# Kernel optimization log

Measured on AMD Instinct MI355X. Metric: run time of the kernel, lower is better.

The kernel has to match this reference:

```python
import jax, jax.numpy as jnp
import numpy as np

NUM_SLOTS = 8
DIM = 256
ITERS = 3
EPS_LN = 1e-5

def _ln(x, g, b):
    mu = jnp.mean(x, axis=-1, keepdims=True)
    var = jnp.var(x, axis=-1, keepdims=True)
    return (x - mu) * jax.lax.rsqrt(var + EPS_LN) * g + b

def setup_inputs() -> dict:
    key = jax.random.key(0)
    ks = jax.random.split(key, 16)
    d = DIM
    s = 1.0 / np.sqrt(d)
    inp = {
        'x': jax.random.normal(ks[0], (64, 4096, d), jnp.float32),
        'noise': jax.random.normal(ks[1], (64, NUM_SLOTS, d), jnp.float32),
        'slots_mu': jax.random.normal(ks[2], (1, 1, d), jnp.float32),
        'slots_logsigma': jnp.zeros((1, 1, d), jnp.float32),
        'Wq': jax.random.uniform(ks[3], (d, d), jnp.float32, -s, s),
        'Wk': jax.random.uniform(ks[4], (d, d), jnp.float32, -s, s),
        'Wv': jax.random.uniform(ks[5], (d, d), jnp.float32, -s, s),
        'W_ih': jax.random.uniform(ks[6], (3 * d, d), jnp.float32, -s, s),
        'W_hh': jax.random.uniform(ks[7], (3 * d, d), jnp.float32, -s, s),
        'b_ih': jax.random.uniform(ks[8], (3 * d,), jnp.float32, -s, s),
        'b_hh': jax.random.uniform(ks[9], (3 * d,), jnp.float32, -s, s),
        'W1': jax.random.uniform(ks[10], (d, d), jnp.float32, -s, s),
        'b1': jax.random.uniform(ks[11], (d,), jnp.float32, -s, s),
        'W2': jax.random.uniform(ks[12], (d, d), jnp.float32, -s, s),
        'b2': jax.random.uniform(ks[13], (d,), jnp.float32, -s, s),
        'g_in': jnp.ones((d,), jnp.float32), 'be_in': jnp.zeros((d,), jnp.float32),
        'g_sl': jnp.ones((d,), jnp.float32), 'be_sl': jnp.zeros((d,), jnp.float32),
        'g_ff': jnp.ones((d,), jnp.float32), 'be_ff': jnp.zeros((d,), jnp.float32),
    }
    return inp

def _gru(x, h, W_ih, W_hh, b_ih, b_hh):
    # torch.nn.GRUCell math; x,h: [M, d]
    gi = x @ W_ih.T + b_ih
    gh = h @ W_hh.T + b_hh
    i_r, i_z, i_n = jnp.split(gi, 3, axis=-1)
    h_r, h_z, h_n = jnp.split(gh, 3, axis=-1)
    r = jax.nn.sigmoid(i_r + h_r)
    z = jax.nn.sigmoid(i_z + h_z)
    n = jnp.tanh(i_n + r * h_n)
    return (1.0 - z) * n + z * h

def reference(x, noise, slots_mu, slots_logsigma, Wq, Wk, Wv, W_ih, W_hh, b_ih, b_hh,
              W1, b1, W2, b2, g_in, be_in, g_sl, be_sl, g_ff, be_ff):
    B, N, d = x.shape
    scale = d ** (-0.5)
    x = _ln(x, g_in, be_in)
    slots = slots_mu + noise * jnp.exp(slots_logsigma)  # [B, K, d]
    # k/v are loop-invariant; hoist (same math as original)
    k = jnp.einsum('bnd,ed->bne', x, Wk)
    v = jnp.einsum('bnd,ed->bne', x, Wv)
    for _ in range(ITERS):
        slots_prev = slots
        q = jnp.einsum('bkd,ed->bke', _ln(slots, g_sl, be_sl), Wq)
        attn = jax.nn.softmax(jnp.einsum('bkd,bnd->bkn', q, k) * scale, axis=-1) + 1e-8
        attn = attn / jnp.sum(attn, axis=-1, keepdims=True)
        updates = jnp.einsum('bkn,bnd->bkd', attn, v)
        slots = _gru(updates.reshape(-1, d), slots_prev.reshape(-1, d),
                     W_ih, W_hh, b_ih, b_hh).reshape(B, NUM_SLOTS, d)
        h = jax.nn.relu(jnp.einsum('bkd,ed->bke', _ln(slots, g_ff, be_ff), W1) + b1)
        slots = slots + jnp.einsum('bkd,ed->bke', h, W2) + b2
    return slots.reshape(B, NUM_SLOTS * d)
```

## Files before the change

### kernel.cpp

```cpp
#include <hip/hip_runtime.h>
#include <cstddef>

#define DIM 256
#define NSLOT 8
#define BATCH 64
#define NTOK 4096
#define SEGB 16
#define NPART SEGB
#define ITERS 3
#define EPS 1e-5f

typedef short bf16x8 __attribute__((ext_vector_type(8)));
typedef short bf16x4 __attribute__((ext_vector_type(4)));
typedef float f32x4  __attribute__((ext_vector_type(4)));

static __device__ __forceinline__ short f2bf(float f) {
    union { float f; unsigned u; } v; v.f = f;
    unsigned r = v.u + 0x7fffu + ((v.u >> 16) & 1u);
    return (short)(r >> 16);
}

enum : size_t {
    OFF_M     = 0,
    OFF_WIHT  = OFF_M    + 256 * 256,
    OFF_WHHT  = OFF_WIHT + 256 * 768,
    OFF_WVT   = OFF_WHHT + 256 * 768,
    OFF_W1T   = OFF_WVT  + 256 * 256,
    OFF_W2T   = OFF_W1T  + 256 * 256,
    OFF_SLOTS = OFF_W2T  + 256 * 256,
    OFF_SNEW  = OFF_SLOTS + BATCH * NSLOT * 256,
    OFF_QT    = OFF_SNEW  + BATCH * NSLOT * 256,
    OFF_H     = OFF_QT    + BATCH * NSLOT * 256,
    OFF_UPD   = OFF_H     + BATCH * NSLOT * 256,
    OFF_UPART = OFF_UPD   + BATCH * NSLOT * 256,
    OFF_LPART = OFF_UPART + (size_t)BATCH * NPART * NSLOT * 256,
    OFF_XLN   = OFF_LPART + BATCH * NPART * 16,
    OFF_XLT   = OFF_XLN   + (size_t)BATCH * NTOK * 128,
    WS_FLOATS = OFF_XLT   + (size_t)BATCH * NTOK * 128
};

__global__ __launch_bounds__(256) void k_transpose(const float* __restrict__ w_ih,
                                                   const float* __restrict__ w_hh,
                                                   const float* __restrict__ wv,
                                                   const float* __restrict__ w1,
                                                   const float* __restrict__ w2,
                                                   float* __restrict__ ws) {
    int z = blockIdx.z;
    const float* src;
    float* dst;
    int R;
    if (z == 0)      { src = w_ih; dst = ws + OFF_WIHT; R = 768; }
    else if (z == 1) { src = w_hh; dst = ws + OFF_WHHT; R = 768; }
    else if (z == 2) { src = wv;   dst = ws + OFF_WVT;  R = 256; }
    else if (z == 3) { src = w1;   dst = ws + OFF_W1T;  R = 256; }
    else             { src = w2;   dst = ws + OFF_W2T;  R = 256; }
    if ((int)blockIdx.x * 32 >= R) return;
    __shared__ float tile[32][33];
    int lx = threadIdx.x & 31, ly = threadIdx.x >> 5;
    int r0 = blockIdx.x * 32, c0 = blockIdx.y * 32;
#pragma unroll
    for (int p = 0; p < 4; ++p)
        tile[ly + p * 8][lx] = src[(size_t)(r0 + ly + p * 8) * 256 + c0 + lx];
    __syncthreads();
#pragma unroll
    for (int p = 0; p < 4; ++p)
        dst[(size_t)(c0 + ly + p * 8) * R + r0 + lx] = tile[lx][ly + p * 8];
}

__global__ __launch_bounds__(256) void k_m(const float* __restrict__ wq,
                                           const float* __restrict__ wk,
                                           float* __restrict__ ws) {
    int d = blockIdx.x, t = threadIdx.x;
    float acc = 0.f;
    for (int e = 0; e < 256; ++e)
        acc += wq[e * 256 + d] * wk[e * 256 + t];
    ws[OFF_M + d * 256 + t] = acc * 0.0625f;
}

__global__ __launch_bounds__(256) void k_init(const float* __restrict__ mu,
                                              const float* __restrict__ logsig,
                                              const float* __restrict__ noise,
                                              float* __restrict__ ws) {
    int i = blockIdx.x * 256 + threadIdx.x;
    int d = i & 255;
    ws[OFF_SLOTS + i] = mu[d] + noise[i] * __expf(logsig[d]);
}

__global__ __launch_bounds__(256) void k_prep(const float* __restrict__ x,
                                              const float* __restrict__ g_in,
                                              const float* __restrict__ be_in,
                                              float* __restrict__ ws) {
    int seg = blockIdx.x, b = blockIdx.y;
    int t = threadIdx.x;
    int w = t >> 6, lane = t & 63;
    int q = lane >> 4, s16 = lane & 15;

    __shared__ short xT[256 * 64];
    __shared__ float gl[256], bl[256];
    gl[t] = g_in[t];
    bl[t] = be_in[t];
    __syncthreads();

    short* xln = (short*)(ws + OFF_XLN);
    short* xlt = (short*)(ws + OFF_XLT);
    int g0 = ((w * 16 + s16) >> 3);
    int t7 = s16 & 7;

    for (int tt = 0; tt < 4; ++tt) {
        int tok = seg * 256 + tt * 64 + w * 16 + s16;
        const float4* xp = (const float4*)(x + ((size_t)b * NTOK + tok) * 256 + q * 8);
        float4 xa[8], xb[8];
#pragma unroll
        for (int i = 0; i < 8; ++i) { xa[i] = xp[8 * i]; xb[i] = xp[8 * i + 1]; }
        float s1 = 0.f, s2 = 0.f;
#pragma unroll
        for (int i = 0; i < 8; ++i) {
            s1 += xa[i].x + xa[i].y + xa[i].z + xa[i].w + xb[i].x + xb[i].y + xb[i].z + xb[i].w;
            s2 += xa[i].x * xa[i].x + xa[i].y * xa[i].y + xa[i].z * xa[i].z + xa[i].w * xa[i].w
                + xb[i].x * xb[i].x + xb[i].y * xb[i].y + xb[i].z * xb[i].z + xb[i].w * xb[i].w;
        }
        s1 += __shfl_xor(s1, 16); s2 += __shfl_xor(s2, 16);
        s1 += __shfl_xor(s1, 32); s2 += __shfl_xor(s2, 32);
        float mu = s1 * (1.f / 256.f);
        float rstd = rsqrtf(s2 * (1.f / 256.f) - mu * mu + EPS);

        bf16x8 af[8];
#pragma unroll
        for (int i = 0; i < 8; ++i) {
            int dbase = i * 32 + q * 8;
            float4 gA = *(const float4*)&gl[dbase];
            float4 gB = *(const float4*)&gl[dbase + 4];
            float4 bA = *(const float4*)&bl[dbase];
            float4 bB = *(const float4*)&bl[dbase + 4];
            bf16x8 f;
            f[0] = f2bf((xa[i].x - mu) * rstd * gA.x + bA.x);
            f[1] = f2bf((xa[i].y - mu) * rstd * gA.y + bA.y);
            f[2] = f2bf((xa[i].z - mu) * rstd * gA.z + bA.z);
            f[3] = f2bf((xa[i].w - mu) * rstd * gA.w + bA.w);
            f[4] = f2bf((xb[i].x - mu) * rstd * gB.x + bB.x);
            f[5] = f2bf((xb[i].y - mu) * rstd * gB.y + bB.y);
            f[6] = f2bf((xb[i].z - mu) * rstd * gB.z + bB.z);
            f[7] = f2bf((xb[i].w - mu) * rstd * gB.w + bB.w);
            af[i] = f;
        }

        short* xrow = xln + ((size_t)b * NTOK + tok) * 256;
#pragma unroll
        for (int i = 0; i < 8; ++i)
            *(bf16x8*)&xrow[i * 32 + q * 8] = af[i];

        __syncthreads();

#pragma unroll
        for (int i = 0; i < 8; ++i) {
            int Ki = (4 * i + q) & 7;
            int dbase = i * 32 + q * 8;
            bf16x8 f = af[i];
#pragma unroll
            for (int e = 0; e < 8; ++e) {
                int gp = (g0 ^ e ^ Ki) & 7;
                xT[((dbase + e) << 6) + (gp << 3) + t7] = f[e];
            }
        }
        __syncthreads();

        short* xtb = xlt + (size_t)(b * 64 + seg * 4 + tt) * 256 * 64;
#pragma unroll
        for (int c = 0; c < 4; ++c) {
            int d = (4 * w + c) * 16 + s16;
            int swz = (d ^ (d >> 3)) & 7;
            const short* row = &xT[d << 6];
            bf16x8 b0 = *(const bf16x8*)&row[((q ^ swz) & 7) << 3];
            bf16x8 b1 = *(const bf16x8*)&row[(((4 + q) ^ swz) & 7) << 3];
            *(bf16x8*)&xtb[d * 64 + q * 8] = b0;
            *(bf16x8*)&xtb[d * 64 + (q + 4) * 8] = b1;
        }
    }
}

__global__ __launch_bounds__(256) void k_qt(float* __restrict__ ws,
                                            const float* __restrict__ g_sl,
                                            const float* __restrict__ be_sl) {
    __shared__ float ln[2048];
    int chunk = blockIdx.x, b = blockIdx.y;
    int t = threadIdx.x, wave = t >> 6, lane = t & 63;
    const float* slots = ws + OFF_SLOTS + b * 2048;
    float4 gf = ((const float4*)g_sl)[lane];
    float4 bf = ((const float4*)be_sl)[lane];
#pragma unroll
    for (int rr = 0; rr < 2; ++rr) {
        int r = wave + rr * 4;
        float4 v = ((const float4*)(slots + r * 256))[lane];
        float s1 = v.x + v.y + v.z + v.w;
        float s2 = v.x * v.x + v.y * v.y + v.z * v.z + v.w * v.w;
#pragma unroll
        for (int m = 1; m < 64; m <<= 1) { s1 += __shfl_xor(s1, m); s2 += __shfl_xor(s2, m); }
        float mu = s1 * (1.f / 256.f);
        float rstd = rsqrtf(s2 * (1.f / 256.f) - mu * mu + EPS);
        float4 o;
        o.x = (v.x - mu) * rstd * gf.x + bf.x;
        o.y = (v.y - mu) * rstd * gf.y + bf.y;
        o.z = (v.z - mu) * rstd * gf.z + bf.z;
        o.w = (v.w - mu) * rstd * gf.w + bf.w;
        *((float4*)&ln[r * 256 + lane * 4]) = o;
    }
    __syncthreads();
    const float* M = ws + OFF_M;
    int k0 = t >> 6;
    int e = chunk * 64 + (t & 63);
    float a0 = 0.f, a1 = 0.f;
    for (int d = 0; d < 256; ++d) {
        float m = M[d * 256 + e];
        a0 += ln[k0 * 256 + d] * m;
        a1 += ln[(k0 + 4) * 256 + d] * m;
    }
    float* qt = ws + OFF_QT + b * 2048;
    qt[k0 * 256 + e] = a0;
    qt[(k0 + 4) * 256 + e] = a1;
}

__global__ __launch_bounds__(256) void k_attn(float* __restrict__ ws) {
    int seg = blockIdx.x, b = blockIdx.y;
    int t = threadIdx.x;
    int w = t >> 6, lane = t & 63;
    int q = lane >> 4, s16 = lane & 15;

    __shared__ short qhi[16 * 264];
    __shared__ short Etmp[2][16 * 72];
    __shared__ float lsum[4][8];

    const float* qtg = ws + OFF_QT + b * 2048;
    for (int idx = t; idx < 16 * 264; idx += 256) {
        int s = idx / 264, d = idx - s * 264;
        qhi[idx] = (s < 8 && d < 256) ? f2bf(qtg[s * 256 + d]) : (short)0;
    }
    __syncthreads();

    bf16x8 qf[8];
#pragma unroll
    for (int i = 0; i < 8; ++i)
        qf[i] = *(const bf16x8*)&qhi[s16 * 264 + i * 32 + q * 8];

    f32x4 U[4];
#pragma unroll
    for (int c = 0; c < 4; ++c) U[c] = (f32x4){0.f, 0.f, 0.f, 0.f};
    float lacc = 0.f;

    const short* xln = (const short*)(ws + OFF_XLN);
    const short* xlt = (const short*)(ws + OFF_XLT);
    int mytok = seg * 256 + w * 16 + s16;

    for (int tt = 0; tt < 4; ++tt) {
        const short* xr = xln + ((size_t)b * NTOK + mytok + tt * 64) * 256 + q * 8;
        bf16x8 af[8];
#pragma unroll
        for (int i = 0; i < 8; ++i) af[i] = *(const bf16x8*)&xr[i * 32];

        f32x4 Lc = (f32x4){0.f, 0.f, 0.f, 0.f};
#pragma unroll
        for (int i = 0; i < 8; ++i)
            Lc = __builtin_amdgcn_mfma_f32_16x16x32_bf16(af[i], qf[i], Lc, 0, 0, 0);

        bf16x4 e2;
#pragma unroll
        for (int r = 0; r < 4; ++r) {
            float E = __expf(fminf(Lc[r], 30.f));
            lacc += E;
            e2[r] = f2bf(E);
        }
        *(bf16x4*)&Etmp[tt & 1][s16 * 72 + w * 16 + q * 4] = e2;
        __syncthreads();

        bf16x8 ea0 = *(const bf16x8*)&Etmp[tt & 1][s16 * 72 + q * 8];
        bf16x8 ea1 = *(const bf16x8*)&Etmp[tt & 1][s16 * 72 + 32 + q * 8];

        const short* xtb = xlt + (size_t)(b * 64 + seg * 4 + tt) * 256 * 64;
#pragma unroll
        for (int c = 0; c < 4; ++c) {
            int d = (4 * w + c) * 16 + s16;
            bf16x8 b0 = *(const bf16x8*)&xtb[d * 64 + q * 8];
            bf16x8 b1 = *(const bf16x8*)&xtb[d * 64 + (q + 4) * 8];
            U[c] = __builtin_amdgcn_mfma_f32_16x16x32_bf16(ea0, b0, U[c], 0, 0, 0);
            U[c] = __builtin_amdgcn_mfma_f32_16x16x32_bf16(ea1, b1, U[c], 0, 0, 0);
        }
    }

    lacc += __shfl_xor(lacc, 16); lacc += __shfl_xor(lacc, 32);
    __syncthreads();
    if (q == 0 && s16 < 8) lsum[w][s16] = lacc;
    __syncthreads();
    float* lpart = ws + OFF_LPART + (size_t)(b * NPART + seg) * 16;
    if (t < 8) lpart[t] = lsum[0][t] + lsum[1][t] + lsum[2][t] + lsum[3][t];
    float* up = ws + OFF_UPART + (size_t)(b * NPART + seg) * NSLOT * 256;
#pragma unroll
    for (int c = 0; c < 4; ++c) {
        int d = (4 * w + c) * 16 + s16;
#pragma unroll
        for (int r = 0; r < 4; ++r) {
            int slot = q * 4 + r;
            if (slot < 8) up[slot * 256 + d] = U[c][r];
        }
    }
}

static __device__ __forceinline__ void ln_row2(const float* src, float* dst,
                                               const float* __restrict__ g,
                                               const float* __restrict__ be,
                                               int wave, int lane) {
    if (wave < 2) {
        float4 v = *(const float4*)(src + wave * 256 + lane * 4);
        float s1 = v.x + v.y + v.z + v.w;
        float s2 = v.x * v.x + v.y * v.y + v.z * v.z + v.w * v.w;
#pragma unroll
        for (int m = 1; m < 64; m <<= 1) { s1 += __shfl_xor(s1, m); s2 += __shfl_xor(s2, m); }
        float mu = s1 * (1.f / 256.f);
        float rstd = rsqrtf(s2 * (1.f / 256.f) - mu * mu + EPS);
        float4 gf = ((const float4*)g)[lane];
        float4 bf = ((const float4*)be)[lane];
        float4 o;
        o.x = (v.x - mu) * rstd * gf.x + bf.x;
        o.y = (v.y - mu) * rstd * gf.y + bf.y;
        o.z = (v.z - mu) * rstd * gf.z + bf.z;
        o.w = (v.w - mu) * rstd * gf.w + bf.w;
        *(float4*)(dst + wave * 256 + lane * 4) = o;
    }
}

__global__ __launch_bounds__(512) void k_fused(float* __restrict__ ws,
                                               const float* __restrict__ b_ih,
                                               const float* __restrict__ b_hh,
                                               const float* __restrict__ g_ff,
                                               const float* __restrict__ be_ff,
                                               const float* __restrict__ b1p,
                                               const float* __restrict__ b2p,
                                               const float* __restrict__ g_sl,
                                               const float* __restrict__ be_sl,
                                               float* __restrict__ dout) {
    __shared__ __align__(16) float uc[2][256], upd[2][256], sl[2][256], snew[2][256];
    __shared__ __align__(16) float lnb[2][256], hbuf[2][256], so[2][256];
    __shared__ float lsv[2];

    int sp = blockIdx.x, b = blockIdx.y, t = threadIdx.x;
    int s0 = sp * 2;
    int s = t >> 8, d = t & 255;
    int wave = t >> 6, lane = t & 63;

    if (t < 32) {
        int ss = t >> 4, g = t & 15;
        float lv = ws[OFF_LPART + (size_t)(b * NPART + g) * 16 + s0 + ss];
#pragma unroll
        for (int m = 1; m < 16; m <<= 1) lv += __shfl_xor(lv, m);
        if ((t & 15) == 0) lsv[ss] = lv;
    }

    const float* up0 = ws + OFF_UPART + (size_t)b * NPART * NSLOT * 256 + (s0 + s) * 256 + d;
    float acc = 0.f;
#pragma unroll
    for (int g = 0; g < NPART; ++g) acc += up0[(size_t)g * NSLOT * 256];
    sl[s][d] = ws[OFF_SLOTS + (size_t)b * 2048 + (s0 + s) * 256 + d];
    __syncthreads();
    uc[s][d] = acc / lsv[s];
    __syncthreads();

    {
        const float* WvT = ws + OFF_WVT;
        float o = 0.f;
        for (int dd = 0; dd < 256; ++dd) o += uc[s][dd] * WvT[dd * 256 + d];
        upd[s][d] = o;
    }
    __syncthreads();

    {
        const float* WihT = ws + OFF_WIHT;
        const float* WhhT = ws + OFF_WHHT;
        float ar = 0.f, az = 0.f, an = 0.f, hr = 0.f, hz = 0.f, hn = 0.f;
        for (int dd = 0; dd < 256; ++dd) {
            float ud = upd[s][dd], sd = sl[s][dd];
            const float* wi = WihT + dd * 768;
            const float* wh = WhhT + dd * 768;
            ar += ud * wi[d];       az += ud * wi[256 + d]; an += ud * wi[512 + d];
            hr += sd * wh[d];       hz += sd * wh[256 + d]; hn += sd * wh[512 + d];
        }
        float rg = 1.f / (1.f + __expf(-(ar + b_ih[d] + hr + b_hh[d])));
        float zg = 1.f / (1.f + __expf(-(az + b_ih[256 + d] + hz + b_hh[256 + d])));
        float ng = tanhf(an + b_ih[512 + d] + rg * (hn + b_hh[512 + d]));
        snew[s][d] = (1.f - zg) * ng + zg * sl[s][d];
    }
    __syncthreads();

    ln_row2(&snew[0][0], &lnb[0][0], g_ff, be_ff, wave, lane);
    __syncthreads();

    {
        const float* W1T = ws + OFF_W1T;
        float o = 0.f;
        for (int dd = 0; dd < 256; ++dd) o += lnb[s][dd] * W1T[dd * 256 + d];
        hbuf[s][d] = fmaxf(o + b1p[d], 0.f);
    }
    __syncthreads();

    {
        const float* W2T = ws + OFF_W2T;
        float o = 0.f;
        for (int dd = 0; dd < 256; ++dd) o += hbuf[s][dd] * W2T[dd * 256 + d];
        float r = snew[s][d] + o + b2p[d];
        so[s][d] = r;
        ws[OFF_SLOTS + (size_t)b * 2048 + (s0 + s) * 256 + d] = r;
        if (dout) dout[(size_t)b * 2048 + (s0 + s) * 256 + d] = r;
    }

    if (!dout) {
        __syncthreads();
        ln_row2(&so[0][0], &lnb[0][0], g_sl, be_sl, wave, lane);
        __syncthreads();
        const float* M = ws + OFF_M;
        float o = 0.f;
        for (int dd = 0; dd < 256; ++dd) o += lnb[s][dd] * M[dd * 256 + d];
        ws[OFF_QT + (size_t)b * 2048 + (s0 + s) * 256 + d] = o;
    }
}

extern "C" void kernel_launch(void* const* d_in, const int* in_sizes, int n_in,
                              void* d_out, int out_size, void* d_ws, size_t ws_size,
                              hipStream_t stream) {
    const float* x      = (const float*)d_in[0];
    const float* noise  = (const float*)d_in[1];
    const float* mu     = (const float*)d_in[2];
    const float* logsig = (const float*)d_in[3];
    const float* Wq     = (const float*)d_in[4];
    const float* Wk     = (const float*)d_in[5];
    const float* Wv     = (const float*)d_in[6];
    const float* W_ih   = (const float*)d_in[7];
    const float* W_hh   = (const float*)d_in[8];
    const float* b_ih   = (const float*)d_in[9];
    const float* b_hh   = (const float*)d_in[10];
    const float* W1     = (const float*)d_in[11];
    const float* b1     = (const float*)d_in[12];
    const float* W2     = (const float*)d_in[13];
    const float* b2     = (const float*)d_in[14];
    const float* g_in   = (const float*)d_in[15];
    const float* be_in  = (const float*)d_in[16];
    const float* g_sl   = (const float*)d_in[17];
    const float* be_sl  = (const float*)d_in[18];
    const float* g_ff   = (const float*)d_in[19];
    const float* be_ff  = (const float*)d_in[20];
    float* ws = (float*)d_ws;
    float* out = (float*)d_out;

    hipLaunchKernelGGL(k_transpose, dim3(24, 8, 5), dim3(256), 0, stream, W_ih, W_hh, Wv, W1, W2, ws);
    hipLaunchKernelGGL(k_m, dim3(256), dim3(256), 0, stream, Wq, Wk, ws);
    hipLaunchKernelGGL(k_init, dim3(512), dim3(256), 0, stream, mu, logsig, noise, ws);
    hipLaunchKernelGGL(k_prep, dim3(SEGB, 64), dim3(256), 0, stream, x, g_in, be_in, ws);
    hipLaunchKernelGGL(k_qt, dim3(4, 64), dim3(256), 0, stream, ws, g_sl, be_sl);
    for (int it = 0; it < ITERS; ++it) {
        hipLaunchKernelGGL(k_attn, dim3(SEGB, 64), dim3(256), 0, stream, ws);
        hipLaunchKernelGGL(k_fused, dim3(4, 64), dim3(512), 0, stream, ws,
                           b_ih, b_hh, g_ff, be_ff, b1, b2, g_sl, be_sl,
                           (it == ITERS - 1) ? out : nullptr);
    }
}
```

Before: 837.1 us.

## Fuse input layernorm into first attention pass and transpose x in LDS

Removes the separate prep kernel and the stored transposed copy of the normalized input. The first attention iteration normalizes x itself and writes the bf16 row-major copy. Every iteration now builds the transposed tile in shared memory instead of reading a second global buffer, which halves the bf16 traffic per pass. It also prefetches the next tile's rows and splits the score MFMA chain into two accumulators, at the cost of more LDS work, an extra barrier per tile, and higher register pressure.

```diff
diff --git a/kernel.cpp b/kernel.cpp
--- a/kernel.cpp
+++ b/kernel.cpp
@@ -35,8 +35,7 @@
     OFF_UPART = OFF_UPD   + BATCH * NSLOT * 256,
     OFF_LPART = OFF_UPART + (size_t)BATCH * NPART * NSLOT * 256,
     OFF_XLN   = OFF_LPART + BATCH * NPART * 16,
-    OFF_XLT   = OFF_XLN   + (size_t)BATCH * NTOK * 128,
-    WS_FLOATS = OFF_XLT   + (size_t)BATCH * NTOK * 128
+    WS_FLOATS = OFF_XLN   + (size_t)BATCH * NTOK * 128
 };
 
 __global__ __launch_bounds__(256) void k_transpose(const float* __restrict__ w_ih,
@@ -86,98 +85,6 @@
     ws[OFF_SLOTS + i] = mu[d] + noise[i] * __expf(logsig[d]);
 }
 
-__global__ __launch_bounds__(256) void k_prep(const float* __restrict__ x,
-                                              const float* __restrict__ g_in,
-                                              const float* __restrict__ be_in,
-                                              float* __restrict__ ws) {
-    int seg = blockIdx.x, b = blockIdx.y;
-    int t = threadIdx.x;
-    int w = t >> 6, lane = t & 63;
-    int q = lane >> 4, s16 = lane & 15;
-
-    __shared__ short xT[256 * 64];
-    __shared__ float gl[256], bl[256];
-    gl[t] = g_in[t];
-    bl[t] = be_in[t];
-    __syncthreads();
-
-    short* xln = (short*)(ws + OFF_XLN);
-    short* xlt = (short*)(ws + OFF_XLT);
-    int g0 = ((w * 16 + s16) >> 3);
-    int t7 = s16 & 7;
-
-    for (int tt = 0; tt < 4; ++tt) {
-        int tok = seg * 256 + tt * 64 + w * 16 + s16;
-        const float4* xp = (const float4*)(x + ((size_t)b * NTOK + tok) * 256 + q * 8);
-        float4 xa[8], xb[8];
-#pragma unroll
-        for (int i = 0; i < 8; ++i) { xa[i] = xp[8 * i]; xb[i] = xp[8 * i + 1]; }
-        float s1 = 0.f, s2 = 0.f;
-#pragma unroll
-        for (int i = 0; i < 8; ++i) {
-            s1 += xa[i].x + xa[i].y + xa[i].z + xa[i].w + xb[i].x + xb[i].y + xb[i].z + xb[i].w;
-            s2 += xa[i].x * xa[i].x + xa[i].y * xa[i].y + xa[i].z * xa[i].z + xa[i].w * xa[i].w
-                + xb[i].x * xb[i].x + xb[i].y * xb[i].y + xb[i].z * xb[i].z + xb[i].w * xb[i].w;
-        }
-        s1 += __shfl_xor(s1, 16); s2 += __shfl_xor(s2, 16);
-        s1 += __shfl_xor(s1, 32); s2 += __shfl_xor(s2, 32);
-        float mu = s1 * (1.f / 256.f);
-        float rstd = rsqrtf(s2 * (1.f / 256.f) - mu * mu + EPS);
-
-        bf16x8 af[8];
-#pragma unroll
-        for (int i = 0; i < 8; ++i) {
-            int dbase = i * 32 + q * 8;
-            float4 gA = *(const float4*)&gl[dbase];
-            float4 gB = *(const float4*)&gl[dbase + 4];
-            float4 bA = *(const float4*)&bl[dbase];
-            float4 bB = *(const float4*)&bl[dbase + 4];
-            bf16x8 f;
-            f[0] = f2bf((xa[i].x - mu) * rstd * gA.x + bA.x);
-            f[1] = f2bf((xa[i].y - mu) * rstd * gA.y + bA.y);
-            f[2] = f2bf((xa[i].z - mu) * rstd * gA.z + bA.z);
-            f[3] = f2bf((xa[i].w - mu) * rstd * gA.w + bA.w);
-            f[4] = f2bf((xb[i].x - mu) * rstd * gB.x + bB.x);
-            f[5] = f2bf((xb[i].y - mu) * rstd * gB.y + bB.y);
-            f[6] = f2bf((xb[i].z - mu) * rstd * gB.z + bB.z);
-            f[7] = f2bf((xb[i].w - mu) * rstd * gB.w + bB.w);
-            af[i] = f;
-        }
-
-        short* xrow = xln + ((size_t)b * NTOK + tok) * 256;
-#pragma unroll
-        for (int i = 0; i < 8; ++i)
-            *(bf16x8*)&xrow[i * 32 + q * 8] = af[i];
-
-        __syncthreads();
-
-#pragma unroll
-        for (int i = 0; i < 8; ++i) {
-            int Ki = (4 * i + q) & 7;
-            int dbase = i * 32 + q * 8;
-            bf16x8 f = af[i];
-#pragma unroll
-            for (int e = 0; e < 8; ++e) {
-                int gp = (g0 ^ e ^ Ki) & 7;
-                xT[((dbase + e) << 6) + (gp << 3) + t7] = f[e];
-            }
-        }
-        __syncthreads();
-
-        short* xtb = xlt + (size_t)(b * 64 + seg * 4 + tt) * 256 * 64;
-#pragma unroll
-        for (int c = 0; c < 4; ++c) {
-            int d = (4 * w + c) * 16 + s16;
-            int swz = (d ^ (d >> 3)) & 7;
-            const short* row = &xT[d << 6];
-            bf16x8 b0 = *(const bf16x8*)&row[((q ^ swz) & 7) << 3];
-            bf16x8 b1 = *(const bf16x8*)&row[(((4 + q) ^ swz) & 7) << 3];
-            *(bf16x8*)&xtb[d * 64 + q * 8] = b0;
-            *(bf16x8*)&xtb[d * 64 + (q + 4) * 8] = b1;
-        }
-    }
-}
-
 __global__ __launch_bounds__(256) void k_qt(float* __restrict__ ws,
                                             const float* __restrict__ g_sl,
                                             const float* __restrict__ be_sl) {
@@ -219,69 +126,150 @@
     qt[(k0 + 4) * 256 + e] = a1;
 }
 
-__global__ __launch_bounds__(256) void k_attn(float* __restrict__ ws) {
+template <bool P1>
+__global__ __launch_bounds__(256) void k_attn_t(const float* __restrict__ x,
+                                                const float* __restrict__ g_in,
+                                                const float* __restrict__ be_in,
+                                                float* __restrict__ ws) {
     int seg = blockIdx.x, b = blockIdx.y;
     int t = threadIdx.x;
     int w = t >> 6, lane = t & 63;
     int q = lane >> 4, s16 = lane & 15;
 
-    __shared__ short qhi[16 * 264];
-    __shared__ short Etmp[2][16 * 72];
+    __shared__ short qhi[8 * 264];
+    __shared__ short xT[256 * 64];
+    __shared__ short Etmp[16 * 72];
     __shared__ float lsum[4][8];
 
     const float* qtg = ws + OFF_QT + b * 2048;
-    for (int idx = t; idx < 16 * 264; idx += 256) {
-        int s = idx / 264, d = idx - s * 264;
-        qhi[idx] = (s < 8 && d < 256) ? f2bf(qtg[s * 256 + d]) : (short)0;
+    for (int idx = t; idx < 8 * 264; idx += 256) {
+        int s = idx >> 8;
+        s = idx / 264;
+        int d = idx - s * 264;
+        qhi[idx] = (d < 256) ? f2bf(qtg[s * 256 + d]) : (short)0;
     }
     __syncthreads();
 
     bf16x8 qf[8];
 #pragma unroll
-    for (int i = 0; i < 8; ++i)
-        qf[i] = *(const bf16x8*)&qhi[s16 * 264 + i * 32 + q * 8];
+    for (int i = 0; i < 8; ++i) {
+        if (s16 < 8) qf[i] = *(const bf16x8*)&qhi[s16 * 264 + i * 32 + q * 8];
+        else         qf[i] = (bf16x8){0, 0, 0, 0, 0, 0, 0, 0};
+    }
 
     f32x4 U[4];
 #pragma unroll
     for (int c = 0; c < 4; ++c) U[c] = (f32x4){0.f, 0.f, 0.f, 0.f};
     float lacc = 0.f;
 
-    const short* xln = (const short*)(ws + OFF_XLN);
-    const short* xlt = (const short*)(ws + OFF_XLT);
+    short* xln = (short*)(ws + OFF_XLN);
     int mytok = seg * 256 + w * 16 + s16;
+    int g0 = ((w * 16 + s16) >> 3);
+    int t7 = s16 & 7;
+
+    bf16x8 af[8];
+    if (!P1) {
+        const short* xr = xln + ((size_t)b * NTOK + mytok) * 256 + q * 8;
+#pragma unroll
+        for (int i = 0; i < 8; ++i) af[i] = *(const bf16x8*)&xr[i * 32];
+    }
 
     for (int tt = 0; tt < 4; ++tt) {
-        const short* xr = xln + ((size_t)b * NTOK + mytok + tt * 64) * 256 + q * 8;
-        bf16x8 af[8];
-#pragma unroll
-        for (int i = 0; i < 8; ++i) af[i] = *(const bf16x8*)&xr[i * 32];
-
-        f32x4 Lc = (f32x4){0.f, 0.f, 0.f, 0.f};
-#pragma unroll
-        for (int i = 0; i < 8; ++i)
-            Lc = __builtin_amdgcn_mfma_f32_16x16x32_bf16(af[i], qf[i], Lc, 0, 0, 0);
+        int tok = mytok + tt * 64;
+        if (P1) {
+            const float4* xp = (const float4*)(x + ((size_t)b * NTOK + tok) * 256 + q * 8);
+            float4 xa[8], xb[8];
+#pragma unroll
+            for (int i = 0; i < 8; ++i) { xa[i] = xp[8 * i]; xb[i] = xp[8 * i + 1]; }
+            float s1 = 0.f, s2 = 0.f;
+#pragma unroll
+            for (int i = 0; i < 8; ++i) {
+                s1 += xa[i].x + xa[i].y + xa[i].z + xa[i].w + xb[i].x + xb[i].y + xb[i].z + xb[i].w;
+                s2 += xa[i].x * xa[i].x + xa[i].y * xa[i].y + xa[i].z * xa[i].z + xa[i].w * xa[i].w
+                    + xb[i].x * xb[i].x + xb[i].y * xb[i].y + xb[i].z * xb[i].z + xb[i].w * xb[i].w;
+            }
+            s1 += __shfl_xor(s1, 16); s2 += __shfl_xor(s2, 16);
+            s1 += __shfl_xor(s1, 32); s2 += __shfl_xor(s2, 32);
+            float mu = s1 * (1.f / 256.f);
+            float rstd = rsqrtf(s2 * (1.f / 256.f) - mu * mu + EPS);
+            short* xrow = xln + ((size_t)b * NTOK + tok) * 256;
+#pragma unroll
+            for (int i = 0; i < 8; ++i) {
+                int dbase = i * 32 + q * 8;
+                float4 gA = *(const float4*)&g_in[dbase];
+                float4 gB = *(const float4*)&g_in[dbase + 4];
+                float4 bA = *(const float4*)&be_in[dbase];
+                float4 bB = *(const float4*)&be_in[dbase + 4];
+                bf16x8 f;
+                f[0] = f2bf((xa[i].x - mu) * rstd * gA.x + bA.x);
+                f[1] = f2bf((xa[i].y - mu) * rstd * gA.y + bA.y);
+                f[2] = f2bf((xa[i].z - mu) * rstd * gA.z + bA.z);
+                f[3] = f2bf((xa[i].w - mu) * rstd * gA.w + bA.w);
+                f[4] = f2bf((xb[i].x - mu) * rstd * gB.x + bB.x);
+                f[5] = f2bf((xb[i].y - mu) * rstd * gB.y + bB.y);
+                f[6] = f2bf((xb[i].z - mu) * rstd * gB.z + bB.z);
+                f[7] = f2bf((xb[i].w - mu) * rstd * gB.w + bB.w);
+                af[i] = f;
+                *(bf16x8*)&xrow[i * 32 + q * 8] = f;
+            }
+        }
+
+        f32x4 Lc0 = (f32x4){0.f, 0.f, 0.f, 0.f};
+        f32x4 Lc1 = (f32x4){0.f, 0.f, 0.f, 0.f};
+#pragma unroll
+        for (int i = 0; i < 4; ++i) {
+            Lc0 = __builtin_amdgcn_mfma_f32_16x16x32_bf16(af[i],     qf[i],     Lc0, 0, 0, 0);
+            Lc1 = __builtin_amdgcn_mfma_f32_16x16x32_bf16(af[i + 4], qf[i + 4], Lc1, 0, 0, 0);
+        }
 
         bf16x4 e2;
 #pragma unroll
         for (int r = 0; r < 4; ++r) {
-            float E = __expf(fminf(Lc[r], 30.f));
+            float E = __expf(fminf(Lc0[r] + Lc1[r], 30.f));
             lacc += E;
             e2[r] = f2bf(E);
         }
-        *(bf16x4*)&Etmp[tt & 1][s16 * 72 + w * 16 + q * 4] = e2;
+
         __syncthreads();
 
-        bf16x8 ea0 = *(const bf16x8*)&Etmp[tt & 1][s16 * 72 + q * 8];
-        bf16x8 ea1 = *(const bf16x8*)&Etmp[tt & 1][s16 * 72 + 32 + q * 8];
-
-        const short* xtb = xlt + (size_t)(b * 64 + seg * 4 + tt) * 256 * 64;
+#pragma unroll
+        for (int i = 0; i < 8; ++i) {
+            int Ki = (4 * i + q) & 7;
+            int dbase = i * 32 + q * 8;
+            bf16x8 f = af[i];
+#pragma unroll
+            for (int e = 0; e < 8; ++e) {
+                int gp = (g0 ^ e ^ Ki) & 7;
+                xT[((dbase + e) << 6) + (gp << 3) + t7] = f[e];
+            }
+        }
+        *(bf16x4*)&Etmp[s16 * 72 + w * 16 + q * 4] = e2;
+
+        __syncthreads();
+
+        bf16x8 afn[8];
+        if (!P1 && tt < 3) {
+            const short* xr = xln + ((size_t)b * NTOK + tok + 64) * 256 + q * 8;
+#pragma unroll
+            for (int i = 0; i < 8; ++i) afn[i] = *(const bf16x8*)&xr[i * 32];
+        }
+
+        bf16x8 ea0 = *(const bf16x8*)&Etmp[s16 * 72 + q * 8];
+        bf16x8 ea1 = *(const bf16x8*)&Etmp[s16 * 72 + 32 + q * 8];
 #pragma unroll
         for (int c = 0; c < 4; ++c) {
             int d = (4 * w + c) * 16 + s16;
-            bf16x8 b0 = *(const bf16x8*)&xtb[d * 64 + q * 8];
-            bf16x8 b1 = *(const bf16x8*)&xtb[d * 64 + (q + 4) * 8];
+            int swz = (d ^ (d >> 3)) & 7;
+            const short* row = &xT[d << 6];
+            bf16x8 b0 = *(const bf16x8*)&row[((q ^ swz) & 7) << 3];
+            bf16x8 b1 = *(const bf16x8*)&row[(((4 + q) ^ swz) & 7) << 3];
             U[c] = __builtin_amdgcn_mfma_f32_16x16x32_bf16(ea0, b0, U[c], 0, 0, 0);
             U[c] = __builtin_amdgcn_mfma_f32_16x16x32_bf16(ea1, b1, U[c], 0, 0, 0);
+        }
+
+        if (!P1 && tt < 3) {
+#pragma unroll
+            for (int i = 0; i < 8; ++i) af[i] = afn[i];
         }
     }
 
@@ -450,10 +438,12 @@
     hipLaunchKernelGGL(k_transpose, dim3(24, 8, 5), dim3(256), 0, stream, W_ih, W_hh, Wv, W1, W2, ws);
     hipLaunchKernelGGL(k_m, dim3(256), dim3(256), 0, stream, Wq, Wk, ws);
     hipLaunchKernelGGL(k_init, dim3(512), dim3(256), 0, stream, mu, logsig, noise, ws);
-    hipLaunchKernelGGL(k_prep, dim3(SEGB, 64), dim3(256), 0, stream, x, g_in, be_in, ws);
     hipLaunchKernelGGL(k_qt, dim3(4, 64), dim3(256), 0, stream, ws, g_sl, be_sl);
     for (int it = 0; it < ITERS; ++it) {
-        hipLaunchKernelGGL(k_attn, dim3(SEGB, 64), dim3(256), 0, stream, ws);
+        if (it == 0)
+            hipLaunchKernelGGL((k_attn_t<true>),  dim3(SEGB, 64), dim3(256), 0, stream, x, g_in, be_in, ws);
+        else
+            hipLaunchKernelGGL((k_attn_t<false>), dim3(SEGB, 64), dim3(256), 0, stream, x, g_in, be_in, ws);
         hipLaunchKernelGGL(k_fused, dim3(4, 64), dim3(512), 0, stream, ws,
                            b_ih, b_hh, g_ff, be_ff, b1, b2, g_sl, be_sl,
                            (it == ITERS - 1) ? out : nullptr);
```

New measurement: 732.0 us. 1.14x faster.
